# Kernel tuning notes

Hardware: AMD Instinct MI355X
Metric: run time of the kernel (lower is better)

The kernel has to match this reference:

```python
import jax, jax.numpy as jnp
import numpy as np

D, H, DK, DF = 512, 8, 64, 2048  # dim, heads, head_dim, forward_dim
EPS = 1e-5


def _layernorm(x, g, b):
    mu = jnp.mean(x, axis=-1, keepdims=True)
    var = jnp.mean(jnp.square(x - mu), axis=-1, keepdims=True)
    return (x - mu) * jax.lax.rsqrt(var + EPS) * g + b


def setup_inputs() -> dict:
    key = jax.random.key(0)
    ks = jax.random.split(key, 16)
    B, S = 2, 2048
    s_in = 1.0 / np.sqrt(D)
    s_ff = 1.0 / np.sqrt(DF)
    s_cat = 1.0 / np.sqrt(H * DK)
    return {
        "x": jax.random.normal(ks[0], (B, S, D), jnp.float32),
        # per-head Q/K/V projections stacked over heads: [H, D, DK]
        "Wq": jax.random.uniform(ks[1], (H, D, DK), jnp.float32, -s_in, s_in),
        "bq": jax.random.uniform(ks[2], (H, DK), jnp.float32, -s_in, s_in),
        "Wk": jax.random.uniform(ks[3], (H, D, DK), jnp.float32, -s_in, s_in),
        "bk": jax.random.uniform(ks[4], (H, DK), jnp.float32, -s_in, s_in),
        "Wv": jax.random.uniform(ks[5], (H, D, DK), jnp.float32, -s_in, s_in),
        "bv": jax.random.uniform(ks[6], (H, DK), jnp.float32, -s_in, s_in),
        "Wo": jax.random.uniform(ks[7], (H * DK, D), jnp.float32, -s_cat, s_cat),
        "bo": jax.random.uniform(ks[8], (D,), jnp.float32, -s_cat, s_cat),
        "ln1_g": jnp.ones((D,), jnp.float32),
        "ln1_b": jnp.zeros((D,), jnp.float32),
        "W1": jax.random.uniform(ks[9], (D, DF), jnp.float32, -s_in, s_in),
        "b1": jax.random.uniform(ks[10], (DF,), jnp.float32, -s_in, s_in),
        "W2": jax.random.uniform(ks[11], (DF, D), jnp.float32, -s_ff, s_ff),
        "b2": jax.random.uniform(ks[12], (D,), jnp.float32, -s_ff, s_ff),
        "ln2_g": jnp.ones((D,), jnp.float32),
        "ln2_b": jnp.zeros((D,), jnp.float32),
    }


def reference(x, Wq, bq, Wk, bk, Wv, bv, Wo, bo, ln1_g, ln1_b, W1, b1, W2, b2, ln2_g, ln2_b):
    # Per-head projections, batched over heads: [B,H,S,DK]
    q = jnp.einsum('bsd,hdk->bhsk', x, Wq) + bq[None, :, None, :]
    k = jnp.einsum('bsd,hdk->bhsk', x, Wk) + bk[None, :, None, :]
    v = jnp.einsum('bsd,hdk->bhsk', x, Wv) + bv[None, :, None, :]
    scale = 1.0 / np.sqrt(DK)
    scores = jnp.einsum('bhsk,bhtk->bhst', q, k) * scale  # [B,H,S,S]
    attn = jax.nn.softmax(scores, axis=-1)
    o = jnp.einsum('bhst,bhtk->bhsk', attn, v)  # [B,H,S,DK]
    # concat heads (head order matches torch cat over ModuleList)
    B, _, S, _ = o.shape
    o = o.transpose(0, 2, 1, 3).reshape(B, S, H * DK)
    attn_out = o @ Wo + bo
    # Residual 1 (dropout = identity in eval): LN(x + sublayer(x))
    h = _layernorm(x + attn_out, ln1_g, ln1_b)
    # FeedForward + Residual 2
    ff = jax.nn.relu(h @ W1 + b1) @ W2 + b2
    return _layernorm(h + ff, ln2_g, ln2_b)
```

## Files before the change

### kernel.cpp

```cpp
#include <hip/hip_runtime.h>


#define Dm   512
#define Hh   8
#define DKk  64
#define DFf  2048
#define Bb   2
#define Ss   2048
#define Nn   4096

typedef __attribute__((ext_vector_type(8))) short short8;
typedef __attribute__((ext_vector_type(4))) float f32x4;
typedef __attribute__((ext_vector_type(4))) short short4v;
typedef __attribute__((ext_vector_type(2))) int   int2v;

__device__ inline float bf2f(short s) {
    unsigned u = ((unsigned)(unsigned short)s) << 16;
    float f; __builtin_memcpy(&f, &u, 4); return f;
}
__device__ inline short f2bf(float f) {
    unsigned u; __builtin_memcpy(&u, &f, 4);
    u = (u + 0x7fff + ((u >> 16) & 1)) >> 16;
    return (short)u;
}
__device__ inline short cvt_elem(const void* p, long i, int f32flag) {
    if (f32flag) return f2bf(((const float*)p)[i]);
    return ((const short*)p)[i];
}
__device__ inline int detect_f32(const void* x) {
    const float* xf = (const float*)x;
    int ok = 0;
#pragma unroll
    for (int i = 0; i < 16; ++i) {
        float a = fabsf(xf[i]);
        ok += (a > 1e-8f && a < 1e4f) ? 1 : 0;
    }
    return ok >= 8;
}
__device__ inline void gload_lds16(const short* g, short* l) {
    __builtin_amdgcn_global_load_lds(
        (const __attribute__((address_space(1))) unsigned int*)g,
        (__attribute__((address_space(3))) unsigned int*)l, 16, 0, 0);
}

__global__ __launch_bounds__(256) void prep_kernel(
    const void* __restrict__ x, short* __restrict__ xb,
    const void* bq, const void* bk, const void* bv, const void* bo,
    const void* b1, const void* b2, const void* g1, const void* be1,
    const void* g2, const void* be2, short* __restrict__ smalls,
    const void* Wq, const void* Wk, const void* Wv,
    const void* Wo, const void* W1, const void* W2,
    short* __restrict__ WqkvT,
    short* __restrict__ WoT, short* __restrict__ W1T, short* __restrict__ W2T)
{
    const int f = detect_f32(x);
    int blk = blockIdx.x;
    if (blk < 512) {
        long base = (long)blk * 4096;
        for (int i = threadIdx.x; i < 4096; i += 256)
            xb[base + i] = cvt_elem(x, base + i, f);
        return;
    }
    if (blk == 512) {
        const void* srcs[10] = {bq, bk, bv, bo, b1, b2, g1, be1, g2, be2};
        const int   sz[10]   = {512, 512, 512, 512, 2048, 512, 512, 512, 512, 512};
        int off = 0;
        for (int j = 0; j < 10; ++j) {
            for (int i = threadIdx.x; i < sz[j]; i += 256)
                smalls[off + i] = cvt_elem(srcs[j], i, f);
            off += sz[j];
        }
        return;
    }
    __shared__ short tile[64][65];
    blk -= 513;
    const void* src; short* dst; long srcoff = 0; long dstoff = 0; int R, C, tr, tc;
    if (blk < 192) {
        int m = blk >> 6; int r = blk & 63; int h = r >> 3; int t = r & 7;
        src = (m == 0) ? Wq : (m == 1) ? Wk : Wv;
        dst = WqkvT + (long)m * 512 * 512;
        srcoff = (long)h * 512 * 64; dstoff = (long)h * 64 * 512;
        R = 512; C = 64; tr = t; tc = 0;
    } else if (blk < 256) {
        int r = blk - 192; src = Wo; dst = WoT; R = 512; C = 512; tr = r >> 3; tc = r & 7;
    } else if (blk < 512) {
        int r = blk - 256; src = W1; dst = W1T; R = 512; C = 2048; tr = r >> 5; tc = r & 31;
    } else {
        int r = blk - 512; src = W2; dst = W2T; R = 2048; C = 512; tr = r >> 3; tc = r & 7;
    }
    int r0 = tr * 64, c0 = tc * 64;
    for (int i = threadIdx.x; i < 4096; i += 256) {
        int rr = i >> 6, cc = i & 63;
        tile[rr][cc] = cvt_elem(src, srcoff + (long)(r0 + rr) * C + c0 + cc, f);
    }
    __syncthreads();
    for (int i = threadIdx.x; i < 4096; i += 256) {
        int cc = i >> 6, rr = i & 63;
        dst[dstoff + (long)(c0 + cc) * R + r0 + rr] = tile[rr][cc];
    }
}

#define MODE_F32       1
#define MODE_RELU_BF16 2
#define MODE_QKV       4

__global__ __launch_bounds__(256) void gemm_kernel(
    const short* __restrict__ A, const short* __restrict__ Bt,
    const short* __restrict__ bias, void* __restrict__ outp,
    void* __restrict__ out2, void* __restrict__ out3,
    int K, int Ncols, int mode, int Ktile)
{
    __shared__ short As[2][128 * 64];
    __shared__ short Bs[2][128 * 64];
    const int t    = threadIdx.x;
    const int lane = t & 63;
    const int wave = t >> 6;
    const int quad = lane >> 4;
    const int l15  = lane & 15;
    const int wm = wave >> 1, wn = wave & 1;
    const int row0 = blockIdx.x * 128;
    const int col0 = blockIdx.y * 128;
    const int kbase = blockIdx.z * Ktile;

    const int ri = lane >> 3;
    const int ct = (lane & 7) ^ ri;

    f32x4 acc[4][4];
#pragma unroll
    for (int i = 0; i < 4; ++i)
#pragma unroll
        for (int j = 0; j < 4; ++j) acc[i][j] = (f32x4){0.f, 0.f, 0.f, 0.f};

    auto stage = [&](int buf, int k0) {
#pragma unroll
        for (int p = 0; p < 4; ++p) {
            int r = wave * 32 + p * 8;
            gload_lds16(A + (long)(row0 + r + ri) * K + kbase + k0 + ct * 8,
                        &As[buf][r * 64 + lane * 8]);
        }
#pragma unroll
        for (int p = 0; p < 4; ++p) {
            int r = wave * 32 + p * 8;
            gload_lds16(Bt + (long)(col0 + r + ri) * K + kbase + k0 + ct * 8,
                        &Bs[buf][r * 64 + lane * 8]);
        }
    };

    stage(0, 0);
    int cur = 0;
    const int niter = Ktile >> 6;
    for (int it = 0; it < niter; ++it) {
        asm volatile("s_waitcnt vmcnt(0)" ::: "memory");
        __syncthreads();
        if (it + 1 < niter) stage(cur ^ 1, (it + 1) * 64);
#pragma unroll
        for (int kk = 0; kk < 2; ++kk) {
            short8 af[4], bfr[4];
#pragma unroll
            for (int mt = 0; mt < 4; ++mt) {
                int rowa = wm * 64 + mt * 16 + l15;
                af[mt] = *(const short8*)&As[cur][rowa * 64
                              + (((kk * 4 + quad) ^ (rowa & 7)) * 8)];
            }
#pragma unroll
            for (int nt = 0; nt < 4; ++nt) {
                int rowb = wn * 64 + nt * 16 + l15;
                bfr[nt] = *(const short8*)&Bs[cur][rowb * 64
                              + (((kk * 4 + quad) ^ (rowb & 7)) * 8)];
            }
#pragma unroll
            for (int mt = 0; mt < 4; ++mt)
#pragma unroll
                for (int nt = 0; nt < 4; ++nt)
                    acc[mt][nt] = __builtin_amdgcn_mfma_f32_16x16x32_bf16(
                        af[mt], bfr[nt], acc[mt][nt], 0, 0, 0);
        }
        cur ^= 1;
    }

    const int wrow0 = row0 + wm * 64;
    const int wcol0 = col0 + wn * 64;
    if (mode == MODE_QKV) {
        int m = wcol0 >> 9;
        if (m < 2) {
            short* out = (short*)(m == 0 ? outp : out2);
            float sc = (m == 0) ? 0.125f : 1.0f;
#pragma unroll
            for (int nt = 0; nt < 4; ++nt) {
                int col = wcol0 + nt * 16 + l15;
                float bb = bf2f(bias[col]);
                int cl = col & 511;
#pragma unroll
                for (int mt = 0; mt < 4; ++mt)
#pragma unroll
                    for (int r = 0; r < 4; ++r) {
                        int row = wrow0 + mt * 16 + quad * 4 + r;
                        out[(long)row * 512 + cl] = f2bf((acc[mt][nt][r] + bb) * sc);
                    }
            }
        } else {
            short* out = (short*)out3;
#pragma unroll
            for (int nt = 0; nt < 4; ++nt) {
                int col = wcol0 + nt * 16 + l15;
                float bb = bf2f(bias[col]);
                int cl = col - 1024;
                int h = cl >> 6, kk = cl & 63;
#pragma unroll
                for (int mt = 0; mt < 4; ++mt)
#pragma unroll
                    for (int r = 0; r < 4; ++r) {
                        int row = wrow0 + mt * 16 + quad * 4 + r;
                        int b = row >> 11, s = row & 2047;
                        out[((long)(b * Hh + h) * DKk + kk) * Ss + s] =
                            f2bf(acc[mt][nt][r] + bb);
                    }
            }
        }
    } else if (mode == MODE_F32) {
        float* out = (float*)outp + (long)blockIdx.z * Nn * Ncols;
        int zb = (blockIdx.z == 0);
#pragma unroll
        for (int nt = 0; nt < 4; ++nt) {
            int col = wcol0 + nt * 16 + l15;
            float bb = zb ? bf2f(bias[col]) : 0.f;
#pragma unroll
            for (int mt = 0; mt < 4; ++mt)
#pragma unroll
                for (int r = 0; r < 4; ++r) {
                    int row = wrow0 + mt * 16 + quad * 4 + r;
                    out[(long)row * Ncols + col] = acc[mt][nt][r] + bb;
                }
        }
    } else {
        short* out = (short*)outp;
#pragma unroll
        for (int nt = 0; nt < 4; ++nt) {
            int col = wcol0 + nt * 16 + l15;
            float bb = bf2f(bias[col]);
#pragma unroll
            for (int mt = 0; mt < 4; ++mt)
#pragma unroll
                for (int r = 0; r < 4; ++r) {
                    int row = wrow0 + mt * 16 + quad * 4 + r;
                    out[(long)row * Ncols + col] = f2bf(fmaxf(acc[mt][nt][r] + bb, 0.f));
                }
        }
    }
}

__global__ __launch_bounds__(256) void attn_kernel(
    const short* __restrict__ Q, const short* __restrict__ Kt,
    const short* __restrict__ Vt, short* __restrict__ po, float* __restrict__ ls)
{
    __shared__ __align__(16) short Ks[64 * 64];
    __shared__ __align__(16) short Vs[64 * 64];
    __shared__ __align__(16) short pbuf[4][32 * 72];
    const int lane = threadIdx.x & 63;
    const int wave = threadIdx.x >> 6;
    const int quad = lane >> 4;
    const int l15  = lane & 15;
    const int qt = blockIdx.x, bh = blockIdx.y, ks = blockIdx.z;
    const int b = bh >> 3, h = bh & 7;
    const int qrow = b * Ss + qt * 128 + wave * 32;

    short8 bq[2][2];
#pragma unroll
    for (int qh = 0; qh < 2; ++qh)
#pragma unroll
        for (int kk = 0; kk < 2; ++kk)
            bq[qh][kk] = *(const short8*)(Q + (long)(qrow + qh * 16 + l15) * Dm
                                          + h * DKk + kk * 32 + quad * 8);

    f32x4 o[2][4];
    float lsum[2] = {0.f, 0.f};
#pragma unroll
    for (int qh = 0; qh < 2; ++qh)
#pragma unroll
        for (int nt = 0; nt < 4; ++nt) o[qh][nt] = (f32x4){0.f, 0.f, 0.f, 0.f};

    const short* Kg = Kt + (long)b * Ss * Dm + h * DKk;
    const short* Vg = Vt + (long)bh * DKk * Ss;
    short* pbw = pbuf[wave];
    const int t00 = ks * 512;

    const int ri = lane >> 3;
    const int ct = (lane & 7) ^ ri;
    const int ldsrow0 = wave * 16;

    for (int it = 0; it < 8; ++it) {
        const int t0 = t00 + it * 64;
#pragma unroll
        for (int p = 0; p < 2; ++p) {
            int r = ldsrow0 + p * 8 + ri;
            gload_lds16(Kg + (long)(t0 + r) * Dm + ct * 8,
                        &Ks[(ldsrow0 + p * 8) * 64] + lane * 8);
        }
#pragma unroll
        for (int p = 0; p < 2; ++p) {
            int r = ldsrow0 + p * 8 + ri;
            gload_lds16(Vg + (long)r * Ss + t0 + ct * 8,
                        &Vs[(ldsrow0 + p * 8) * 64] + lane * 8);
        }
        asm volatile("s_waitcnt vmcnt(0)" ::: "memory");
        __syncthreads();

#pragma unroll
        for (int j = 0; j < 4; ++j) {
            short8 kf0 = *(const short8*)&Ks[(j * 16 + l15) * 64
                                             + ((quad ^ (l15 & 7)) * 8)];
            short8 kf1 = *(const short8*)&Ks[(j * 16 + l15) * 64
                                             + (((4 + quad) ^ (l15 & 7)) * 8)];
#pragma unroll
            for (int qh = 0; qh < 2; ++qh) {
                f32x4 sj = (f32x4){0.f, 0.f, 0.f, 0.f};
                sj = __builtin_amdgcn_mfma_f32_16x16x32_bf16(kf0, bq[qh][0], sj, 0, 0, 0);
                sj = __builtin_amdgcn_mfma_f32_16x16x32_bf16(kf1, bq[qh][1], sj, 0, 0, 0);
                int2v pk;
#pragma unroll
                for (int r2 = 0; r2 < 2; ++r2) {
                    float pa = __expf(fminf(sj[r2 * 2 + 0], 20.f));
                    float pc = __expf(fminf(sj[r2 * 2 + 1], 20.f));
                    lsum[qh] += pa + pc;
                    unsigned ua, uc;
                    __builtin_memcpy(&ua, &pa, 4);
                    __builtin_memcpy(&uc, &pc, 4);
                    pk[r2] = __builtin_amdgcn_perm(uc, ua, 0x07060302);
                }
                *(int2v*)&pbw[(qh * 16 + l15) * 72 + j * 16 + quad * 4] = pk;
            }
        }
        asm volatile("s_waitcnt lgkmcnt(0)" ::: "memory");
#pragma unroll
        for (int c = 0; c < 2; ++c) {
            short8 ap[2];
#pragma unroll
            for (int qh = 0; qh < 2; ++qh)
                ap[qh] = *(const short8*)&pbw[(qh * 16 + l15) * 72 + c * 32 + quad * 8];
#pragma unroll
            for (int nt = 0; nt < 4; ++nt) {
                short8 vf = *(const short8*)&Vs[(nt * 16 + l15) * 64
                                                + (((c * 4 + quad) ^ (l15 & 7)) * 8)];
#pragma unroll
                for (int qh = 0; qh < 2; ++qh)
                    o[qh][nt] = __builtin_amdgcn_mfma_f32_16x16x32_bf16(
                        ap[qh], vf, o[qh][nt], 0, 0, 0);
            }
        }
        asm volatile("" ::: "memory");
        __syncthreads();
    }

#pragma unroll
    for (int qh = 0; qh < 2; ++qh) {
        float v = lsum[qh];
        v += __shfl_xor(v, 16);
        v += __shfl_xor(v, 32);
        lsum[qh] = v;
    }
    short* pob = po + ((((long)bh * 16 + qt) * 4 + ks) * 128) * 64;
#pragma unroll
    for (int qh = 0; qh < 2; ++qh)
#pragma unroll
        for (int nt = 0; nt < 4; ++nt)
#pragma unroll
            for (int r = 0; r < 4; ++r)
                pob[(wave * 32 + qh * 16 + quad * 4 + r) * 64 + nt * 16 + l15] =
                    f2bf(o[qh][nt][r]);
    if (lane < 16) {
        long lbase = (((long)bh * 16 + qt) * 4 + ks) * 128 + wave * 32;
        ls[lbase + l15]      = lsum[0];
        ls[lbase + 16 + l15] = lsum[1];
    }
}

__global__ __launch_bounds__(256) void combine_kernel(
    const short* __restrict__ po, const float* __restrict__ ls,
    short* __restrict__ O)
{
    const int qt = blockIdx.x, bh = blockIdx.y;
    const int b = bh >> 3, h = bh & 7;
    const long base = ((long)bh * 16 + qt) * 4;
    const int tid = threadIdx.x;
    const int qloc = tid >> 4;
    const int dk0 = (tid & 15) * 4;
#pragma unroll
    for (int q0 = 0; q0 < 8; ++q0) {
        int q = q0 * 16 + qloc;
        f32x4 s = (f32x4){0.f, 0.f, 0.f, 0.f};
        float L = 0.f;
#pragma unroll
        for (int ksp = 0; ksp < 4; ++ksp) {
            short4v pv = *(const short4v*)(po + ((base + ksp) * 128 + q) * 64 + dk0);
#pragma unroll
            for (int i = 0; i < 4; ++i) s[i] += bf2f(pv[i]);
            L += ls[(base + ksp) * 128 + q];
        }
        float inv = 1.f / L;
        short4v ov;
#pragma unroll
        for (int i = 0; i < 4; ++i) ov[i] = f2bf(s[i] * inv);
        *(short4v*)(O + (long)(b * Ss + qt * 128 + q) * Dm + h * DKk + dk0) = ov;
    }
}

__global__ __launch_bounds__(256) void ln_kernel(
    const float* __restrict__ v0, const float* __restrict__ v1,
    const float* __restrict__ v2, const float* __restrict__ v3,
    const short* __restrict__ res,
    const short* __restrict__ g, const short* __restrict__ bt,
    void* __restrict__ out, const void* __restrict__ xdet)
{
    const int row = blockIdx.x, tid = threadIdx.x;
    const long base = (long)row * Dm;
    const long i0 = base + tid, i1 = base + 256 + tid;
    float x0 = v0[i0] + bf2f(res[i0]);
    float x1 = v0[i1] + bf2f(res[i1]);
    if (v1) { x0 += v1[i0]; x1 += v1[i1]; }
    if (v2) { x0 += v2[i0]; x1 += v2[i1]; }
    if (v3) { x0 += v3[i0]; x1 += v3[i1]; }

    __shared__ float red[8];
    const int wv = tid >> 6, ln = tid & 63;
    float s = x0 + x1;
#pragma unroll
    for (int mk = 1; mk < 64; mk <<= 1) s += __shfl_xor(s, mk);
    if (!ln) red[wv] = s;
    __syncthreads();
    float mean = (red[0] + red[1] + red[2] + red[3]) * (1.f / 512.f);
    float d0 = x0 - mean, d1 = x1 - mean;
    float q = d0 * d0 + d1 * d1;
#pragma unroll
    for (int mk = 1; mk < 64; mk <<= 1) q += __shfl_xor(q, mk);
    if (!ln) red[4 + wv] = q;
    __syncthreads();
    float rs = rsqrtf((red[4] + red[5] + red[6] + red[7]) * (1.f / 512.f) + 1e-5f);
    float y0 = d0 * rs * bf2f(g[tid])       + bf2f(bt[tid]);
    float y1 = d1 * rs * bf2f(g[256 + tid]) + bf2f(bt[256 + tid]);
    int f32out = xdet ? detect_f32(xdet) : 0;
    if (f32out) {
        float* o = (float*)out;
        o[i0] = y0; o[i1] = y1;
    } else {
        short* o = (short*)out;
        o[i0] = f2bf(y0); o[i1] = f2bf(y1);
    }
}

extern "C" void kernel_launch(void* const* d_in, const int* in_sizes, int n_in,
                              void* d_out, int out_size, void* d_ws, size_t ws_size,
                              hipStream_t stream)
{
    (void)in_sizes; (void)n_in; (void)out_size; (void)ws_size;
    const void* x   = d_in[0];
    const void* Wq  = d_in[1];  const void* bq  = d_in[2];
    const void* Wk  = d_in[3];  const void* bk  = d_in[4];
    const void* Wv  = d_in[5];  const void* bv  = d_in[6];
    const void* Wo  = d_in[7];  const void* bo  = d_in[8];
    const void* g1  = d_in[9];  const void* be1 = d_in[10];
    const void* W1  = d_in[11]; const void* b1  = d_in[12];
    const void* W2  = d_in[13]; const void* b2  = d_in[14];
    const void* g2  = d_in[15]; const void* be2 = d_in[16];

    char* ws = (char*)d_ws;
    size_t off = 0;
    auto alloc = [&](size_t bytes) -> void* {
        void* p = ws + off; off += (bytes + 255) & ~(size_t)255; return p;
    };
    short* WqkvT = (short*)alloc((size_t)3 * Dm * Dm * 2);
    short* WoT   = (short*)alloc((size_t)Dm * Dm * 2);
    short* W1T   = (short*)alloc((size_t)DFf * Dm * 2);
    short* W2T   = (short*)alloc((size_t)Dm * DFf * 2);
    short* xb    = (short*)alloc((size_t)Nn * Dm * 2);
    short* sm    = (short*)alloc((size_t)6656 * 2);
    char*  regA  = (char*)alloc((size_t)Nn * DFf * 2);
    short* Qb    = (short*)(regA);
    short* Kb    = (short*)(regA + (size_t)Nn * Dm * 2);
    short* Vt    = (short*)(regA + (size_t)Nn * Dm * 4);
    short* Ob    = (short*)(regA + (size_t)Nn * Dm * 6);
    short* u     = (short*)(regA);
    float* wo_p  = (float*)alloc((size_t)2 * Nn * Dm * 4);
    char*  regC  = (char*)alloc((size_t)4 * Nn * Dm * 4);
    short* po    = (short*)regC;
    float* f2p   = (float*)regC;
    float* lsb   = (float*)alloc((size_t)16 * 16 * 4 * 128 * 4);
    short* h_bf  = (short*)alloc((size_t)Nn * Dm * 2);

    prep_kernel<<<1281, 256, 0, stream>>>(x, xb, bq, bk, bv, bo, b1, b2,
                                          g1, be1, g2, be2, sm,
                                          Wq, Wk, Wv, Wo, W1, W2,
                                          WqkvT, WoT, W1T, W2T);
    gemm_kernel<<<dim3(Nn / 128, 1536 / 128, 1), 256, 0, stream>>>(
        xb, WqkvT, sm + 0, Qb, Kb, Vt, Dm, 1536, MODE_QKV, Dm);
    attn_kernel<<<dim3(Ss / 128, Bb * Hh, 4), 256, 0, stream>>>(Qb, Kb, Vt, po, lsb);
    combine_kernel<<<dim3(Ss / 128, Bb * Hh), 256, 0, stream>>>(po, lsb, Ob);
    gemm_kernel<<<dim3(Nn / 128, Dm / 128, 2), 256, 0, stream>>>(
        Ob, WoT, sm + 1536, wo_p, nullptr, nullptr, Dm, Dm, MODE_F32, Dm / 2);
    ln_kernel<<<Nn, 256, 0, stream>>>(wo_p, wo_p + (long)Nn * Dm, nullptr, nullptr,
                                      xb, sm + 4608, sm + 5120, h_bf, nullptr);
    gemm_kernel<<<dim3(Nn / 128, DFf / 128, 1), 256, 0, stream>>>(
        h_bf, W1T, sm + 2048, u, nullptr, nullptr, Dm, DFf, MODE_RELU_BF16, Dm);
    gemm_kernel<<<dim3(Nn / 128, Dm / 128, 4), 256, 0, stream>>>(
        u, W2T, sm + 4096, f2p, nullptr, nullptr, DFf, Dm, MODE_F32, DFf / 4);
    ln_kernel<<<Nn, 256, 0, stream>>>(f2p, f2p + (long)Nn * Dm, f2p + (long)2 * Nn * Dm,
                                      f2p + (long)3 * Nn * Dm,
                                      h_bf, sm + 5632, sm + 6144, d_out, x);
}
```

Before: 209.1 us.

## Fuse split-K attention combine into Wo GEMM and vectorize prep/V-transpose stores

```diff
diff --git a/kernel.cpp b/kernel.cpp
--- a/kernel.cpp
+++ b/kernel.cpp
@@ -57,8 +57,14 @@
     int blk = blockIdx.x;
     if (blk < 512) {
         long base = (long)blk * 4096;
-        for (int i = threadIdx.x; i < 4096; i += 256)
-            xb[base + i] = cvt_elem(x, base + i, f);
+        if (!f) {
+            const short8* src8 = (const short8*)((const short*)x + base);
+            short8* dst8 = (short8*)(xb + base);
+            for (int i = threadIdx.x; i < 512; i += 256) dst8[i] = src8[i];
+        } else {
+            for (int i = threadIdx.x; i < 4096; i += 256)
+                xb[base + i] = cvt_elem(x, base + i, f);
+        }
         return;
     }
     if (blk == 512) {
@@ -89,14 +95,32 @@
         int r = blk - 512; src = W2; dst = W2T; R = 2048; C = 512; tr = r >> 3; tc = r & 7;
     }
     int r0 = tr * 64, c0 = tc * 64;
-    for (int i = threadIdx.x; i < 4096; i += 256) {
-        int rr = i >> 6, cc = i & 63;
-        tile[rr][cc] = cvt_elem(src, srcoff + (long)(r0 + rr) * C + c0 + cc, f);
-    }
-    __syncthreads();
-    for (int i = threadIdx.x; i < 4096; i += 256) {
-        int cc = i >> 6, rr = i & 63;
-        dst[dstoff + (long)(c0 + cc) * R + r0 + rr] = tile[rr][cc];
+    if (!f) {
+        const short* s16 = (const short*)src;
+        for (int i = threadIdx.x; i < 512; i += 256) {
+            int rr = i >> 3, c8 = (i & 7) * 8;
+            short8 v = *(const short8*)&s16[srcoff + (long)(r0 + rr) * C + c0 + c8];
+#pragma unroll
+            for (int j = 0; j < 8; ++j) tile[rr][c8 + j] = v[j];
+        }
+        __syncthreads();
+        for (int i = threadIdx.x; i < 512; i += 256) {
+            int cc = i >> 3, r8 = (i & 7) * 8;
+            short8 w;
+#pragma unroll
+            for (int j = 0; j < 8; ++j) w[j] = tile[r8 + j][cc];
+            *(short8*)&dst[dstoff + (long)(c0 + cc) * R + r0 + r8] = w;
+        }
+    } else {
+        for (int i = threadIdx.x; i < 4096; i += 256) {
+            int rr = i >> 6, cc = i & 63;
+            tile[rr][cc] = cvt_elem(src, srcoff + (long)(r0 + rr) * C + c0 + cc, f);
+        }
+        __syncthreads();
+        for (int i = threadIdx.x; i < 4096; i += 256) {
+            int cc = i >> 6, rr = i & 63;
+            dst[dstoff + (long)(c0 + cc) * R + r0 + rr] = tile[rr][cc];
+        }
     }
 }
 
@@ -181,8 +205,8 @@
     const int wrow0 = row0 + wm * 64;
     const int wcol0 = col0 + wn * 64;
     if (mode == MODE_QKV) {
-        int m = wcol0 >> 9;
-        if (m < 2) {
+        if (wcol0 < 1024) {
+            int m = wcol0 >> 9;
             short* out = (short*)(m == 0 ? outp : out2);
             float sc = (m == 0) ? 0.125f : 1.0f;
 #pragma unroll
@@ -199,22 +223,40 @@
                     }
             }
         } else {
+            __syncthreads();
+            short* Asf = &As[0][0];
+#pragma unroll
+            for (int nt = 0; nt < 4; ++nt) {
+                int col_l = wn * 64 + nt * 16 + l15;
+                float bb = bf2f(bias[col0 + col_l]);
+#pragma unroll
+                for (int mt = 0; mt < 4; ++mt) {
+                    int row4 = wm * 16 + mt * 4 + quad;
+                    int slot = row4 ^ (col_l & 31);
+                    short4v pk;
+#pragma unroll
+                    for (int r = 0; r < 4; ++r) pk[r] = f2bf(acc[mt][nt][r] + bb);
+                    *(short4v*)&Asf[col_l * 128 + slot * 4] = pk;
+                }
+            }
+            __syncthreads();
             short* out = (short*)out3;
-#pragma unroll
-            for (int nt = 0; nt < 4; ++nt) {
-                int col = wcol0 + nt * 16 + l15;
-                float bb = bf2f(bias[col]);
-                int cl = col - 1024;
-                int h = cl >> 6, kk = cl & 63;
-#pragma unroll
-                for (int mt = 0; mt < 4; ++mt)
-#pragma unroll
-                    for (int r = 0; r < 4; ++r) {
-                        int row = wrow0 + mt * 16 + quad * 4 + r;
-                        int b = row >> 11, s = row & 2047;
-                        out[((long)(b * Hh + h) * DKk + kk) * Ss + s] =
-                            f2bf(acc[mt][nt][r] + bb);
-                    }
+            int col_l = t >> 1;
+            int cl = col0 + col_l - 1024;
+            int hh = cl >> 6, kk2 = cl & 63;
+            int bg = row0 >> 11;
+            long obase = ((long)(bg * Hh + hh) * DKk + kk2) * Ss + (row0 & 2047);
+#pragma unroll
+            for (int i = 0; i < 8; ++i) {
+                int chunk = (t & 1) * 8 + i;
+                int s0 = (chunk * 2)     ^ (col_l & 31);
+                int s1 = (chunk * 2 + 1) ^ (col_l & 31);
+                short4v a = *(const short4v*)&Asf[col_l * 128 + s0 * 4];
+                short4v b4 = *(const short4v*)&Asf[col_l * 128 + s1 * 4];
+                short8 w;
+                w[0] = a[0];  w[1] = a[1];  w[2] = a[2];  w[3] = a[3];
+                w[4] = b4[0]; w[5] = b4[1]; w[6] = b4[2]; w[7] = b4[3];
+                *(short8*)&out[obase + chunk * 8] = w;
             }
         }
     } else if (mode == MODE_F32) {
@@ -246,6 +288,125 @@
                     out[(long)row * Ncols + col] = f2bf(fmaxf(acc[mt][nt][r] + bb, 0.f));
                 }
         }
+    }
+}
+
+__global__ __launch_bounds__(256) void wogemm_kernel(
+    const short* __restrict__ po, const float* __restrict__ ls,
+    const short* __restrict__ Bt, const short* __restrict__ bias,
+    float* __restrict__ outp)
+{
+    __shared__ short As[2][128 * 64];
+    __shared__ short Bs[2][128 * 64];
+    const int t    = threadIdx.x;
+    const int lane = t & 63;
+    const int wave = t >> 6;
+    const int quad = lane >> 4;
+    const int l15  = lane & 15;
+    const int wm = wave >> 1, wn = wave & 1;
+    const int row0 = blockIdx.x * 128;
+    const int col0 = blockIdx.y * 128;
+    const int z    = blockIdx.z;
+
+    const int ri = lane >> 3;
+    const int ct = (lane & 7) ^ ri;
+    const int myrow = t >> 1;
+    const int tcb = (t & 1) * 4;
+    const int bg = row0 >> 11;
+    const int qtl = (row0 >> 7) & 15;
+
+    f32x4 acc[4][4];
+#pragma unroll
+    for (int i = 0; i < 4; ++i)
+#pragma unroll
+        for (int j = 0; j < 4; ++j) acc[i][j] = (f32x4){0.f, 0.f, 0.f, 0.f};
+
+    auto stageB = [&](int buf, int k0) {
+#pragma unroll
+        for (int p = 0; p < 4; ++p) {
+            int r = wave * 32 + p * 8;
+            gload_lds16(Bt + (long)(col0 + r + ri) * 512 + z * 256 + k0 + ct * 8,
+                        &Bs[buf][r * 64 + lane * 8]);
+        }
+    };
+
+    short8 aR[4][4];
+    float  lR[4];
+    auto loadA = [&](int it) {
+        int h = z * 4 + it;
+        long pbase = ((long)(bg * Hh + h) * 16 + qtl) * 4;
+#pragma unroll
+        for (int ks = 0; ks < 4; ++ks) {
+            lR[ks] = ls[(pbase + ks) * 128 + myrow];
+#pragma unroll
+            for (int c = 0; c < 4; ++c)
+                aR[c][ks] = *(const short8*)&po[((pbase + ks) * 128 + myrow) * 64
+                                                + (tcb + c) * 8];
+        }
+    };
+    auto cvtwrite = [&](int buf) {
+        float invL = __builtin_amdgcn_rcpf(lR[0] + lR[1] + lR[2] + lR[3]);
+#pragma unroll
+        for (int c = 0; c < 4; ++c) {
+            short8 w;
+#pragma unroll
+            for (int j = 0; j < 8; ++j) {
+                float s = bf2f(aR[c][0][j]) + bf2f(aR[c][1][j])
+                        + bf2f(aR[c][2][j]) + bf2f(aR[c][3][j]);
+                w[j] = f2bf(s * invL);
+            }
+            int slot = (tcb + c) ^ (myrow & 7);
+            *(short8*)&As[buf][myrow * 64 + slot * 8] = w;
+        }
+    };
+
+    loadA(0); stageB(0, 0); cvtwrite(0);
+    int cur = 0;
+#pragma unroll
+    for (int it = 0; it < 4; ++it) {
+        __syncthreads();
+        if (it < 3) { loadA(it + 1); stageB(cur ^ 1, (it + 1) * 64); }
+#pragma unroll
+        for (int kk = 0; kk < 2; ++kk) {
+            short8 af[4], bfr[4];
+#pragma unroll
+            for (int mt = 0; mt < 4; ++mt) {
+                int rowa = wm * 64 + mt * 16 + l15;
+                af[mt] = *(const short8*)&As[cur][rowa * 64
+                              + (((kk * 4 + quad) ^ (rowa & 7)) * 8)];
+            }
+#pragma unroll
+            for (int nt = 0; nt < 4; ++nt) {
+                int rowb = wn * 64 + nt * 16 + l15;
+                bfr[nt] = *(const short8*)&Bs[cur][rowb * 64
+                              + (((kk * 4 + quad) ^ (rowb & 7)) * 8)];
+            }
+#pragma unroll
+            for (int mt = 0; mt < 4; ++mt)
+#pragma unroll
+                for (int nt = 0; nt < 4; ++nt)
+                    acc[mt][nt] = __builtin_amdgcn_mfma_f32_16x16x32_bf16(
+                        af[mt], bfr[nt], acc[mt][nt], 0, 0, 0);
+        }
+        if (it < 3) cvtwrite(cur ^ 1);
+        cur ^= 1;
+    }
+
+    const int wrow0 = row0 + wm * 64;
+    const int wcol0 = col0 + wn * 64;
+    float* out = outp + (long)z * Nn * Dm;
+    int zb = (z == 0);
+#pragma unroll
+    for (int nt = 0; nt < 4; ++nt) {
+        int col = wcol0 + nt * 16 + l15;
+        float bb = zb ? bf2f(bias[col]) : 0.f;
+#pragma unroll
+        for (int mt = 0; mt < 4; ++mt)
+#pragma unroll
+            for (int r = 0; r < 4; ++r) {
+                int row = wrow0 + mt * 16 + quad * 4 + r;
+                out[(long)row * Dm + col] = acc[mt][nt][r] + bb;
+            }
     }
 }
 
@@ -371,36 +532,6 @@
         long lbase = (((long)bh * 16 + qt) * 4 + ks) * 128 + wave * 32;
         ls[lbase + l15]      = lsum[0];
         ls[lbase + 16 + l15] = lsum[1];
-    }
-}
-
-__global__ __launch_bounds__(256) void combine_kernel(
-    const short* __restrict__ po, const float* __restrict__ ls,
-    short* __restrict__ O)
-{
-    const int qt = blockIdx.x, bh = blockIdx.y;
-    const int b = bh >> 3, h = bh & 7;
-    const long base = ((long)bh * 16 + qt) * 4;
-    const int tid = threadIdx.x;
-    const int qloc = tid >> 4;
-    const int dk0 = (tid & 15) * 4;
-#pragma unroll
-    for (int q0 = 0; q0 < 8; ++q0) {
-        int q = q0 * 16 + qloc;
-        f32x4 s = (f32x4){0.f, 0.f, 0.f, 0.f};
-        float L = 0.f;
-#pragma unroll
-        for (int ksp = 0; ksp < 4; ++ksp) {
-            short4v pv = *(const short4v*)(po + ((base + ksp) * 128 + q) * 64 + dk0);
-#pragma unroll
-            for (int i = 0; i < 4; ++i) s[i] += bf2f(pv[i]);
-            L += ls[(base + ksp) * 128 + q];
-        }
-        float inv = 1.f / L;
-        short4v ov;
-#pragma unroll
-        for (int i = 0; i < 4; ++i) ov[i] = f2bf(s[i] * inv);
-        *(short4v*)(O + (long)(b * Ss + qt * 128 + q) * Dm + h * DKk + dk0) = ov;
     }
 }
 
@@ -477,7 +608,6 @@
     short* Qb    = (short*)(regA);
     short* Kb    = (short*)(regA + (size_t)Nn * Dm * 2);
     short* Vt    = (short*)(regA + (size_t)Nn * Dm * 4);
-    short* Ob    = (short*)(regA + (size_t)Nn * Dm * 6);
     short* u     = (short*)(regA);
     float* wo_p  = (float*)alloc((size_t)2 * Nn * Dm * 4);
     char*  regC  = (char*)alloc((size_t)4 * Nn * Dm * 4);
@@ -493,9 +623,8 @@
     gemm_kernel<<<dim3(Nn / 128, 1536 / 128, 1), 256, 0, stream>>>(
         xb, WqkvT, sm + 0, Qb, Kb, Vt, Dm, 1536, MODE_QKV, Dm);
     attn_kernel<<<dim3(Ss / 128, Bb * Hh, 4), 256, 0, stream>>>(Qb, Kb, Vt, po, lsb);
-    combine_kernel<<<dim3(Ss / 128, Bb * Hh), 256, 0, stream>>>(po, lsb, Ob);
-    gemm_kernel<<<dim3(Nn / 128, Dm / 128, 2), 256, 0, stream>>>(
-        Ob, WoT, sm + 1536, wo_p, nullptr, nullptr, Dm, Dm, MODE_F32, Dm / 2);
+    wogemm_kernel<<<dim3(Nn / 128, Dm / 128, 2), 256, 0, stream>>>(
+        po, lsb, WoT, sm + 1536, wo_p);
     ln_kernel<<<Nn, 256, 0, stream>>>(wo_p, wo_p + (long)Nn * Dm, nullptr, nullptr,
                                       xb, sm + 4608, sm + 5120, h_bf, nullptr);
     gemm_kernel<<<dim3(Nn / 128, DFf / 128, 1), 256, 0, stream>>>(
```

New measurement: 209.4 us. About the same (+0.1%).
